# Optimization experiments

Hardware: AMD Instinct MI355X
Metric: run time of the kernel (lower is better)

The kernel has to match this reference:

```python
import jax, jax.numpy as jnp
import numpy as np

N = 16384      # batch (samples / graph nodes)
H = 256        # hid_dim
PRED_LEN = 24


def setup_inputs() -> dict:
    key = jax.random.key(0)
    ks = jax.random.split(key, 9)
    s = 1.0 / np.sqrt(H)  # PyTorch default init bound for GRUCell / Linear(H, 1)
    return {
        "encoder_out": jax.random.normal(ks[0], (N, H), dtype=jnp.float32),
        # input_proj = Linear(1, H): weight [H,1] flattened to [H], bound 1/sqrt(1)=1
        "w_proj": jax.random.uniform(ks[1], (H,), jnp.float32, -1.0, 1.0),
        "b_proj": jax.random.uniform(ks[2], (H,), jnp.float32, -1.0, 1.0),
        # GRUCell weights: [3H, H] ordered (reset, update, new) as in PyTorch
        "W_ih": jax.random.uniform(ks[3], (3 * H, H), jnp.float32, -s, s),
        "b_ih": jax.random.uniform(ks[4], (3 * H,), jnp.float32, -s, s),
        "W_hh": jax.random.uniform(ks[5], (3 * H, H), jnp.float32, -s, s),
        "b_hh": jax.random.uniform(ks[6], (3 * H,), jnp.float32, -s, s),
        # output_layer = Linear(H, 1): weight [1,H] flattened to [H]
        "w_out": jax.random.uniform(ks[7], (H,), jnp.float32, -s, s),
        "b_out": jax.random.uniform(ks[8], (1,), jnp.float32, -s, s),
    }


def reference(encoder_out, w_proj, b_proj, W_ih, b_ih, W_hh, b_hh, w_out, b_out):
    def step(carry, _):
        h, x = carry                       # h: [N,H], x: [N,1] scalar step input
        px = x * w_proj + b_proj           # input_proj(Linear(1,H)) -> [N,H]
        gi = px @ W_ih.T + b_ih            # [N,3H]
        gh = h @ W_hh.T + b_hh             # [N,3H]
        i_r, i_z, i_n = jnp.split(gi, 3, axis=1)
        h_r, h_z, h_n = jnp.split(gh, 3, axis=1)
        r = jax.nn.sigmoid(i_r + h_r)
        z = jax.nn.sigmoid(i_z + h_z)
        n = jnp.tanh(i_n + r * h_n)
        h_new = (1.0 - z) * n + z * h      # PyTorch GRUCell update
        pred = (h_new @ w_out)[:, None] + b_out  # output_layer -> [N,1]
        next_x = jax.lax.stop_gradient(pred)     # matches pred_t.detach()
        return (h_new, next_x), pred[:, 0]

    x0 = jnp.zeros((encoder_out.shape[0], 1), dtype=encoder_out.dtype)  # start token
    _, preds = jax.lax.scan(step, (encoder_out, x0), None, length=PRED_LEN)
    return preds.T  # [N, pred_len]
```

## Files before the change

### kernel.cpp

```cpp
#include <hip/hip_runtime.h>
#include <hip/hip_bf16.h>

#define NS 16384
#define H 256
#define TH 768
#define PRED 24
#define LDA 272
#define WS_NEEDED (425984)

typedef short bf16x8 __attribute__((ext_vector_type(8)));
typedef float floatx4 __attribute__((ext_vector_type(4)));

__device__ __forceinline__ float b2f(unsigned short u) {
    return __uint_as_float(((unsigned int)u) << 16);
}
__device__ __forceinline__ unsigned short f2b(float f) {
    unsigned int u = __float_as_uint(f);
    return (unsigned short)((u + 0x7FFFu + ((u >> 16) & 1u)) >> 16);
}
__device__ __forceinline__ float fsig(float v) {
    return __builtin_amdgcn_rcpf(1.0f + __expf(-v));
}
__device__ __forceinline__ float ftanh(float v) {
    return 1.0f - 2.0f * __builtin_amdgcn_rcpf(1.0f + __expf(2.0f * v));
}

__global__ void prep_proj(const void* __restrict__ WihP, const void* __restrict__ wprojP,
                          const void* __restrict__ bprojP, const void* __restrict__ bihP,
                          const void* __restrict__ bhhP, const void* __restrict__ woutP,
                          const void* __restrict__ boutP,
                          float* __restrict__ u, float* __restrict__ c,
                          float* __restrict__ bhn, float* __restrict__ wo,
                          float* __restrict__ b0) {
    const int j = blockIdx.x;
    const int lane = threadIdx.x;
    unsigned long long bm = __ballot(!(fabsf(b2f(((const unsigned short*)WihP)[lane])) <= 0.25f));
    const bool f32in = (bm != 0ull);

    float su = 0.f, sc = 0.f;
    if (f32in) {
        const float* row = (const float*)WihP + (size_t)j * H;
        const float* wp = (const float*)wprojP;
        const float* bp = (const float*)bprojP;
        for (int k = lane; k < H; k += 64) {
            float w = row[k];
            su = fmaf(w, wp[k], su); sc = fmaf(w, bp[k], sc);
        }
    } else {
        const unsigned short* row = (const unsigned short*)WihP + (size_t)j * H;
        const unsigned short* wp = (const unsigned short*)wprojP;
        const unsigned short* bp = (const unsigned short*)bprojP;
        for (int k = lane; k < H; k += 64) {
            float w = b2f(row[k]);
            su = fmaf(w, b2f(wp[k]), su); sc = fmaf(w, b2f(bp[k]), sc);
        }
    }
    for (int m = 32; m; m >>= 1) { su += __shfl_xor(su, m, 64); sc += __shfl_xor(sc, m, 64); }

    if (lane == 0) {
        float bih = f32in ? ((const float*)bihP)[j] : b2f(((const unsigned short*)bihP)[j]);
        float bhh = f32in ? ((const float*)bhhP)[j] : b2f(((const unsigned short*)bhhP)[j]);
        u[j] = su;
        c[j] = sc + bih + (j < 512 ? bhh : 0.f);
        if (j >= 512) bhn[j - 512] = bhh;
    }
    if (j < H && lane == 1)
        wo[j] = f32in ? ((const float*)woutP)[j] : b2f(((const unsigned short*)woutP)[j]);
    if (j == 0 && lane == 2)
        b0[0] = f32in ? ((const float*)boutP)[0] : b2f(((const unsigned short*)boutP)[0]);
}

__global__ void prep_swz2(const void* __restrict__ WhhP, unsigned short* __restrict__ Wp) {
    const int cidx = blockIdx.x * 256 + threadIdx.x;
    unsigned long long bm = __ballot(!(fabsf(b2f(((const unsigned short*)WhhP)[threadIdx.x & 63])) <= 0.25f));
    const bool f32in = (bm != 0ull);

    const int lane = cidx & 63;
    const int fi   = cidx >> 6;
    const int s    = fi & 1;
    const int g    = (fi >> 1) % 3;
    const int kk   = ((fi >> 1) / 3) & 7;
    const int w    = (fi >> 1) / 24;
    const size_t src = (size_t)(g * 256 + s * 128 + w * 16 + (lane & 15)) * H
                     + kk * 32 + (lane >> 4) * 8;
    unsigned short* dst = Wp + (size_t)cidx * 8;
    if (f32in) {
        const float* sp = (const float*)WhhP + src;
#pragma unroll
        for (int e = 0; e < 8; ++e) dst[e] = f2b(sp[e]);
    } else {
        const unsigned short* sp = (const unsigned short*)WhhP + src;
#pragma unroll
        for (int e = 0; e < 8; ++e) dst[e] = sp[e];
    }
}

__global__ void prep_wof(const float* __restrict__ wo, unsigned short* __restrict__ wf) {
    const int idx = blockIdx.x * 256 + threadIdx.x;
    const int kk   = idx >> 9;
    const int lane = (idx >> 3) & 63;
    const int e    = idx & 7;
    unsigned short v = 0;
    if ((lane & 15) == 0) v = f2b(wo[kk * 32 + (lane >> 4) * 8 + e]);
    wf[idx] = v;
}

__global__ __launch_bounds__(512, 2)
void decode_wr2(const void* __restrict__ encP, const void* __restrict__ WihP,
                const unsigned short* __restrict__ Wp, const unsigned short* __restrict__ wf,
                const float* __restrict__ u, const float* __restrict__ c,
                const float* __restrict__ bhnA, const float* __restrict__ b0A,
                void* __restrict__ outP) {
    __shared__ __align__(16) unsigned short As[2][32 * LDA];
    __shared__ __align__(16) unsigned short Wl[8][6144];
    __shared__ __align__(16) unsigned short Wf[8 * 512];
    __shared__ float pred_out[32][PRED];
    __shared__ int sflag;

    const int tid  = threadIdx.x;
    const int w    = tid >> 6;
    const int lane = tid & 63;
    const int lo   = lane & 15;
    const int quad = lane >> 4;
    const int m0   = blockIdx.x * 32;

    if (tid == 0) sflag = 0;
    __syncthreads();
    if (!(fabsf(b2f(((const unsigned short*)WihP)[tid])) <= 0.25f)) sflag = 1;
    __syncthreads();
    const bool f32in = (sflag != 0);

    const float*          encF = (const float*)encP;
    const unsigned short* encB = (const unsigned short*)encP;

    for (int i = tid; i < 32 * H; i += 512) {
        int r = i >> 8, col = i & 255;
        float hv = f32in ? encF[(size_t)(m0 + r) * H + col] : b2f(encB[(size_t)(m0 + r) * H + col]);
        As[0][r * LDA + col] = f2b(hv);
    }
    for (int i = tid; i < 4096; i += 512) Wf[i] = wf[i];

    float ur[2], uz[2], un[2], cr[2], cz[2], cn[2], bh[2];
#pragma unroll
    for (int s = 0; s < 2; ++s) {
        const int jj = s * 128 + w * 16 + lo;
        ur[s] = u[jj];       uz[s] = u[256 + jj];       un[s] = u[512 + jj];
        cr[s] = c[jj];       cz[s] = c[256 + jj];       cn[s] = c[512 + jj];
        bh[s] = bhnA[jj];
    }
    const float b0 = b0A[0];

    const unsigned short* wp = Wp + (size_t)w * 24576 + lane * 8;
    bf16x8 bW[6][3][2];
#pragma unroll
    for (int kk = 0; kk < 6; ++kk)
#pragma unroll
        for (int g = 0; g < 3; ++g)
#pragma unroll
            for (int s = 0; s < 2; ++s)
                bW[kk][g][s] = *(const bf16x8*)(wp + (size_t)((kk * 3 + g) * 2 + s) * 512);
#pragma unroll
    for (int kk = 6; kk < 8; ++kk)
#pragma unroll
        for (int g = 0; g < 3; ++g)
#pragma unroll
            for (int s = 0; s < 2; ++s) {
                bf16x8 v = *(const bf16x8*)(wp + (size_t)((kk * 3 + g) * 2 + s) * 512);
                *(bf16x8*)&Wl[w][(((kk - 6) * 3 + g) * 2 + s) * 512 + lane * 8] = v;
            }
    __syncthreads();

    int p = 0;
#pragma unroll 1
    for (int t = 0; t < PRED; ++t) {
        floatx4 acc[3][2][2];
        floatx4 woacc[2];
#pragma unroll
        for (int g = 0; g < 3; ++g)
#pragma unroll
            for (int s = 0; s < 2; ++s)
#pragma unroll
                for (int im = 0; im < 2; ++im) acc[g][s][im] = (floatx4){0.f, 0.f, 0.f, 0.f};
        woacc[0] = (floatx4){0.f, 0.f, 0.f, 0.f};
        woacc[1] = (floatx4){0.f, 0.f, 0.f, 0.f};

        const unsigned short* Ap = As[p];
        unsigned short*       An = As[p ^ 1];

#pragma unroll
        for (int kk = 0; kk < 8; ++kk) {
            bf16x8 a[2];
#pragma unroll
            for (int im = 0; im < 2; ++im)
                a[im] = *(const bf16x8*)&Ap[(im * 16 + lo) * LDA + kk * 32 + quad * 8];
            bf16x8 bwv = *(const bf16x8*)&Wf[kk * 512 + lane * 8];
            if (kk < 6) {
#pragma unroll
                for (int g = 0; g < 3; ++g)
#pragma unroll
                    for (int s = 0; s < 2; ++s)
#pragma unroll
                        for (int im = 0; im < 2; ++im)
                            acc[g][s][im] = __builtin_amdgcn_mfma_f32_16x16x32_bf16(
                                a[im], bW[kk][g][s], acc[g][s][im], 0, 0, 0);
            } else {
                bf16x8 b[3][2];
#pragma unroll
                for (int g = 0; g < 3; ++g)
#pragma unroll
                    for (int s = 0; s < 2; ++s)
                        b[g][s] = *(const bf16x8*)&Wl[w][(((kk - 6) * 3 + g) * 2 + s) * 512 + lane * 8];
#pragma unroll
                for (int g = 0; g < 3; ++g)
#pragma unroll
                    for (int s = 0; s < 2; ++s)
#pragma unroll
                        for (int im = 0; im < 2; ++im)
                            acc[g][s][im] = __builtin_amdgcn_mfma_f32_16x16x32_bf16(
                                a[im], b[g][s], acc[g][s][im], 0, 0, 0);
            }
#pragma unroll
            for (int im = 0; im < 2; ++im)
                woacc[im] = __builtin_amdgcn_mfma_f32_16x16x32_bf16(a[im], bwv, woacc[im], 0, 0, 0);
        }

#pragma unroll
        for (int im = 0; im < 2; ++im) {
#pragma unroll
            for (int v = 0; v < 4; ++v) {
                const int row = im * 16 + quad * 4 + v;
                float xv = 0.f;
                if (t > 0) xv = b0 + __shfl(woacc[im][v], quad << 4, 64);
#pragma unroll
                for (int s = 0; s < 2; ++s) {
                    const int jj = s * 128 + w * 16 + lo;
                    const int hofs = row * LDA + jj;
                    const float hold = b2f(Ap[hofs]);
                    float r  = fsig(fmaf(xv, ur[s], cr[s]) + acc[0][s][im][v]);
                    float z  = fsig(fmaf(xv, uz[s], cz[s]) + acc[1][s][im][v]);
                    float n  = ftanh(fmaf(xv, un[s], cn[s]) + r * (acc[2][s][im][v] + bh[s]));
                    float hn = fmaf(z, hold - n, n);
                    An[hofs] = f2b(hn);
                }
                if (w == 0 && lo == 0 && t > 0) pred_out[row][t - 1] = xv;
            }
        }
        __syncthreads();
        p ^= 1;
    }

    if (w == 0) {
        const unsigned short* Ap = As[p];
        floatx4 wa[2];
        wa[0] = (floatx4){0.f, 0.f, 0.f, 0.f};
        wa[1] = (floatx4){0.f, 0.f, 0.f, 0.f};
#pragma unroll
        for (int kk = 0; kk < 8; ++kk) {
            bf16x8 bwv = *(const bf16x8*)&Wf[kk * 512 + lane * 8];
#pragma unroll
            for (int im = 0; im < 2; ++im) {
                bf16x8 a = *(const bf16x8*)&Ap[(im * 16 + lo) * LDA + kk * 32 + quad * 8];
                wa[im] = __builtin_amdgcn_mfma_f32_16x16x32_bf16(a, bwv, wa[im], 0, 0, 0);
            }
        }
        if (lo == 0) {
#pragma unroll
            for (int im = 0; im < 2; ++im)
#pragma unroll
                for (int v = 0; v < 4; ++v)
                    pred_out[im * 16 + quad * 4 + v][PRED - 1] = b0 + wa[im][v];
        }
    }
    __syncthreads();

    for (int i = tid; i < 32 * PRED; i += 512) {
        int row = i / PRED, tt = i % PRED;
        float pr = pred_out[row][tt];
        if (f32in) ((float*)outP)[(size_t)(m0 + row) * PRED + tt] = pr;
        else ((unsigned short*)outP)[(size_t)(m0 + row) * PRED + tt] = f2b(pr);
    }
}

__global__ __launch_bounds__(512, 2)
void decode_all(const void* __restrict__ encP,   const void* __restrict__ wprojP,
                const void* __restrict__ bprojP, const void* __restrict__ WihP,
                const void* __restrict__ bihP,   const void* __restrict__ WhhP,
                const void* __restrict__ bhhP,   const void* __restrict__ woutP,
                const void* __restrict__ boutP,  void* __restrict__ outP) {
    __shared__ __align__(16) unsigned short Asf[64 * LDA];
    __shared__ float u_lds[TH], c_lds[TH];
    __shared__ float bhn_lds[H], wo_lds[H];
    __shared__ float wp_lds[H], bp_lds[H];
    __shared__ float pred_lds[2][64];
    __shared__ int sflag;

    const int tid  = threadIdx.x;
    const int wid  = tid >> 6;
    const int lane = tid & 63;
    const int lo   = lane & 15;
    const int quad = lane >> 4;
    const int rh   = wid & 3;
    const int ch   = wid >> 2;
    const int m0   = blockIdx.x * 64;

    if (tid == 0) sflag = 0;
    __syncthreads();
    if (!(fabsf(b2f(((const unsigned short*)WihP)[tid])) <= 0.25f)) sflag = 1;
    __syncthreads();
    const bool f32in = (sflag != 0);

    const float*          encF = (const float*)encP;
    const unsigned short* encB = (const unsigned short*)encP;
    const unsigned short* WhhB = (const unsigned short*)WhhP;
    const float*          WhhF = (const float*)WhhP;

    if (tid < H) {
        wp_lds[tid] = f32in ? ((const float*)wprojP)[tid] : b2f(((const unsigned short*)wprojP)[tid]);
        bp_lds[tid] = f32in ? ((const float*)bprojP)[tid] : b2f(((const unsigned short*)bprojP)[tid]);
        wo_lds[tid] = f32in ? ((const float*)woutP)[tid]  : b2f(((const unsigned short*)woutP)[tid]);
    }
    __syncthreads();

    for (int j = tid; j < TH; j += 512) {
        float su = 0.f, sc = 0.f;
        if (f32in) {
            const float* row = (const float*)WihP + (size_t)j * H;
            for (int k = 0; k < H; ++k) { float w = row[k]; su = fmaf(w, wp_lds[k], su); sc = fmaf(w, bp_lds[k], sc); }
        } else {
            const unsigned short* row = (const unsigned short*)WihP + (size_t)j * H;
            for (int k = 0; k < H; ++k) { float w = b2f(row[k]); su = fmaf(w, wp_lds[k], su); sc = fmaf(w, bp_lds[k], sc); }
        }
        float bih = f32in ? ((const float*)bihP)[j] : b2f(((const unsigned short*)bihP)[j]);
        float bhh = f32in ? ((const float*)bhhP)[j] : b2f(((const unsigned short*)bhhP)[j]);
        u_lds[j] = su;
        c_lds[j] = sc + bih + (j < 512 ? bhh : 0.f);
        if (j >= 512) bhn_lds[j - 512] = bhh;
    }

    for (int i = tid; i < 64 * H; i += 512) {
        int r = i >> 8, col = i & 255;
        float hv = f32in ? encF[(size_t)(m0 + r) * H + col] : b2f(encB[(size_t)(m0 + r) * H + col]);
        Asf[r * LDA + col] = f2b(hv);
    }
    float hold[8][4];
#pragma unroll
    for (int s = 0; s < 8; ++s)
#pragma unroll
        for (int v = 0; v < 4; ++v) {
            int row = m0 + rh * 16 + quad * 4 + v;
            int jj  = ch * 128 + s * 16 + lo;
            hold[s][v] = f32in ? encF[(size_t)row * H + jj] : b2f(encB[(size_t)row * H + jj]);
        }
    const float b0 = f32in ? ((const float*)boutP)[0] : b2f(((const unsigned short*)boutP)[0]);

    float xm[4] = {0.f, 0.f, 0.f, 0.f};
    __syncthreads();

    const int aBase = (rh * 16 + lo) * LDA;
    const int wCol0 = ch * 128 + lo;

#pragma unroll 1
    for (int t = 0; t < PRED; ++t) {
        floatx4 acc[3][8];
#pragma unroll
        for (int g = 0; g < 3; ++g)
#pragma unroll
            for (int s = 0; s < 8; ++s) acc[g][s] = (floatx4){0.f, 0.f, 0.f, 0.f};

        if (f32in) {
#pragma unroll 1
            for (int kk = 0; kk < 8; ++kk) {
                bf16x8 a = *(const bf16x8*)&Asf[aBase + kk * 32 + quad * 8];
#pragma unroll
                for (int g = 0; g < 3; ++g)
#pragma unroll
                    for (int s = 0; s < 8; ++s) {
                        const float* wr = WhhF + (size_t)(g * 256 + wCol0 + s * 16) * H + kk * 32 + quad * 8;
                        float4 w0 = *(const float4*)wr;
                        float4 w1 = *(const float4*)(wr + 4);
                        bf16x8 b;
                        b[0] = (short)f2b(w0.x); b[1] = (short)f2b(w0.y);
                        b[2] = (short)f2b(w0.z); b[3] = (short)f2b(w0.w);
                        b[4] = (short)f2b(w1.x); b[5] = (short)f2b(w1.y);
                        b[6] = (short)f2b(w1.z); b[7] = (short)f2b(w1.w);
                        acc[g][s] = __builtin_amdgcn_mfma_f32_16x16x32_bf16(a, b, acc[g][s], 0, 0, 0);
                    }
            }
        } else {
#pragma unroll 1
            for (int kk = 0; kk < 8; ++kk) {
                bf16x8 a = *(const bf16x8*)&Asf[aBase + kk * 32 + quad * 8];
#pragma unroll
                for (int g = 0; g < 3; ++g)
#pragma unroll
                    for (int s = 0; s < 8; ++s) {
                        bf16x8 b = *(const bf16x8*)(WhhB + (size_t)(g * 256 + wCol0 + s * 16) * H + kk * 32 + quad * 8);
                        acc[g][s] = __builtin_amdgcn_mfma_f32_16x16x32_bf16(a, b, acc[g][s], 0, 0, 0);
                    }
            }
        }
        __syncthreads();

        float pp[4] = {0.f, 0.f, 0.f, 0.f};
#pragma unroll
        for (int s = 0; s < 8; ++s) {
            const int jj = ch * 128 + s * 16 + lo;
            const float urr = u_lds[jj], uzz = u_lds[256 + jj], unn = u_lds[512 + jj];
            const float crr = c_lds[jj], czz = c_lds[256 + jj], cnn = c_lds[512 + jj];
            const float bhn = bhn_lds[jj], wovv = wo_lds[jj];
#pragma unroll
            for (int v = 0; v < 4; ++v) {
                const float xv = xm[v];
                float r  = fsig(fmaf(xv, urr, crr) + acc[0][s][v]);
                float z  = fsig(fmaf(xv, uzz, czz) + acc[1][s][v]);
                float n  = ftanh(fmaf(xv, unn, cnn) + r * (acc[2][s][v] + bhn));
                float hn = fmaf(z, hold[s][v] - n, n);
                hold[s][v] = hn;
                Asf[(rh * 16 + quad * 4 + v) * LDA + jj] = f2b(hn);
                pp[v] = fmaf(hn, wovv, pp[v]);
            }
        }
#pragma unroll
        for (int v = 0; v < 4; ++v) {
            float pv = pp[v];
            pv += __shfl_xor(pv, 1, 64);
            pv += __shfl_xor(pv, 2, 64);
            pv += __shfl_xor(pv, 4, 64);
            pv += __shfl_xor(pv, 8, 64);
            if (lo == 0) pred_lds[ch][rh * 16 + quad * 4 + v] = pv;
        }
        __syncthreads();

#pragma unroll
        for (int v = 0; v < 4; ++v) {
            const int ml = rh * 16 + quad * 4 + v;
            xm[v] = b0 + pred_lds[0][ml] + pred_lds[1][ml];
        }
        if (tid < 64) {
            float pr = b0 + pred_lds[0][tid] + pred_lds[1][tid];
            if (f32in) ((float*)outP)[(size_t)(m0 + tid) * PRED + t] = pr;
            else ((unsigned short*)outP)[(size_t)(m0 + tid) * PRED + t] = f2b(pr);
        }
    }
}

extern "C" void kernel_launch(void* const* d_in, const int* in_sizes, int n_in,
                              void* d_out, int out_size, void* d_ws, size_t ws_size,
                              hipStream_t stream) {
    if (ws_size >= (size_t)WS_NEEDED) {
        char* ws = (char*)d_ws;
        unsigned short* Wp = (unsigned short*)ws;
        float* u   = (float*)(ws + 393216);
        float* c   = (float*)(ws + 396288);
        float* bhn = (float*)(ws + 399360);
        float* wo  = (float*)(ws + 400384);
        float* b0  = (float*)(ws + 401408);
        unsigned short* wf = (unsigned short*)(ws + 402432);
        prep_proj<<<TH, 64, 0, stream>>>(d_in[3], d_in[1], d_in[2], d_in[4], d_in[6],
                                         d_in[7], d_in[8], u, c, bhn, wo, b0);
        prep_swz2<<<96, 256, 0, stream>>>(d_in[5], Wp);
        prep_wof<<<16, 256, 0, stream>>>(wo, wf);
        decode_wr2<<<NS / 32, 512, 0, stream>>>(d_in[0], d_in[3], Wp, wf, u, c, bhn, b0, d_out);
    } else {
        decode_all<<<NS / 64, 512, 0, stream>>>(d_in[0], d_in[1], d_in[2], d_in[3],
                                                d_in[4], d_in[5], d_in[6], d_in[7],
                                                d_in[8], d_out);
    }
}
```

Baseline: 319.9 us.

## Hold all W_hh in registers with 64-row tiles and fp32 hidden state

The decode kernel now processes 64 rows per block instead of 32 and runs one block per CU. It keeps the full swizzled W_hh slice and the output-weight fragments in registers rather than splitting them between registers and LDS. The previous hidden state is carried in fp32 registers instead of being re-read from the bf16 LDS tile. This doubles the MFMA reuse of each weight fragment and removes the LDS weight traffic, at the cost of heavy register pressure, lower occupancy and only 256 blocks on the device.

```diff
diff --git a/kernel.cpp b/kernel.cpp
--- a/kernel.cpp
+++ b/kernel.cpp
@@ -105,16 +105,14 @@
     wf[idx] = v;
 }
 
-__global__ __launch_bounds__(512, 2)
-void decode_wr2(const void* __restrict__ encP, const void* __restrict__ WihP,
-                const unsigned short* __restrict__ Wp, const unsigned short* __restrict__ wf,
-                const float* __restrict__ u, const float* __restrict__ c,
-                const float* __restrict__ bhnA, const float* __restrict__ b0A,
-                void* __restrict__ outP) {
-    __shared__ __align__(16) unsigned short As[2][32 * LDA];
-    __shared__ __align__(16) unsigned short Wl[8][6144];
-    __shared__ __align__(16) unsigned short Wf[8 * 512];
-    __shared__ float pred_out[32][PRED];
+__global__ __launch_bounds__(512, 1)
+void decode_wf(const void* __restrict__ encP, const void* __restrict__ WihP,
+               const unsigned short* __restrict__ Wp, const unsigned short* __restrict__ wf,
+               const float* __restrict__ u, const float* __restrict__ c,
+               const float* __restrict__ bhnA, const float* __restrict__ b0A,
+               void* __restrict__ outP) {
+    __shared__ __align__(16) unsigned short As[2][64 * LDA];
+    __shared__ float pred_out[64][PRED];
     __shared__ int sflag;
 
     const int tid  = threadIdx.x;
@@ -122,7 +120,7 @@
     const int lane = tid & 63;
     const int lo   = lane & 15;
     const int quad = lane >> 4;
-    const int m0   = blockIdx.x * 32;
+    const int m0   = blockIdx.x * 64;
 
     if (tid == 0) sflag = 0;
     __syncthreads();
@@ -133,12 +131,11 @@
     const float*          encF = (const float*)encP;
     const unsigned short* encB = (const unsigned short*)encP;
 
-    for (int i = tid; i < 32 * H; i += 512) {
+    for (int i = tid; i < 64 * H; i += 512) {
         int r = i >> 8, col = i & 255;
         float hv = f32in ? encF[(size_t)(m0 + r) * H + col] : b2f(encB[(size_t)(m0 + r) * H + col]);
         As[0][r * LDA + col] = f2b(hv);
     }
-    for (int i = tid; i < 4096; i += 512) Wf[i] = wf[i];
 
     float ur[2], uz[2], un[2], cr[2], cz[2], cn[2], bh[2];
 #pragma unroll
@@ -150,82 +147,73 @@
     }
     const float b0 = b0A[0];
 
+    float hold[4][4][2];
+#pragma unroll
+    for (int im = 0; im < 4; ++im)
+#pragma unroll
+        for (int v = 0; v < 4; ++v)
+#pragma unroll
+            for (int s = 0; s < 2; ++s) {
+                int row = m0 + im * 16 + quad * 4 + v;
+                int jj  = s * 128 + w * 16 + lo;
+                hold[im][v][s] = f32in ? encF[(size_t)row * H + jj]
+                                       : b2f(encB[(size_t)row * H + jj]);
+            }
+
     const unsigned short* wp = Wp + (size_t)w * 24576 + lane * 8;
-    bf16x8 bW[6][3][2];
-#pragma unroll
-    for (int kk = 0; kk < 6; ++kk)
+    bf16x8 bW[8][3][2];
+#pragma unroll
+    for (int kk = 0; kk < 8; ++kk)
 #pragma unroll
         for (int g = 0; g < 3; ++g)
 #pragma unroll
             for (int s = 0; s < 2; ++s)
                 bW[kk][g][s] = *(const bf16x8*)(wp + (size_t)((kk * 3 + g) * 2 + s) * 512);
-#pragma unroll
-    for (int kk = 6; kk < 8; ++kk)
-#pragma unroll
-        for (int g = 0; g < 3; ++g)
-#pragma unroll
-            for (int s = 0; s < 2; ++s) {
-                bf16x8 v = *(const bf16x8*)(wp + (size_t)((kk * 3 + g) * 2 + s) * 512);
-                *(bf16x8*)&Wl[w][(((kk - 6) * 3 + g) * 2 + s) * 512 + lane * 8] = v;
-            }
+    bf16x8 bWo[8];
+#pragma unroll
+    for (int kk = 0; kk < 8; ++kk)
+        bWo[kk] = *(const bf16x8*)(wf + kk * 512 + lane * 8);
+
     __syncthreads();
 
     int p = 0;
 #pragma unroll 1
     for (int t = 0; t < PRED; ++t) {
-        floatx4 acc[3][2][2];
-        floatx4 woacc[2];
+        floatx4 acc[3][2][4];
+        floatx4 woacc[4];
 #pragma unroll
         for (int g = 0; g < 3; ++g)
 #pragma unroll
             for (int s = 0; s < 2; ++s)
 #pragma unroll
-                for (int im = 0; im < 2; ++im) acc[g][s][im] = (floatx4){0.f, 0.f, 0.f, 0.f};
-        woacc[0] = (floatx4){0.f, 0.f, 0.f, 0.f};
-        woacc[1] = (floatx4){0.f, 0.f, 0.f, 0.f};
+                for (int im = 0; im < 4; ++im) acc[g][s][im] = (floatx4){0.f, 0.f, 0.f, 0.f};
+#pragma unroll
+        for (int im = 0; im < 4; ++im) woacc[im] = (floatx4){0.f, 0.f, 0.f, 0.f};
 
         const unsigned short* Ap = As[p];
         unsigned short*       An = As[p ^ 1];
 
 #pragma unroll
         for (int kk = 0; kk < 8; ++kk) {
-            bf16x8 a[2];
-#pragma unroll
-            for (int im = 0; im < 2; ++im)
+            bf16x8 a[4];
+#pragma unroll
+            for (int im = 0; im < 4; ++im)
                 a[im] = *(const bf16x8*)&Ap[(im * 16 + lo) * LDA + kk * 32 + quad * 8];
-            bf16x8 bwv = *(const bf16x8*)&Wf[kk * 512 + lane * 8];
-            if (kk < 6) {
-#pragma unroll
-                for (int g = 0; g < 3; ++g)
-#pragma unroll
-                    for (int s = 0; s < 2; ++s)
-#pragma unroll
-                        for (int im = 0; im < 2; ++im)
-                            acc[g][s][im] = __builtin_amdgcn_mfma_f32_16x16x32_bf16(
-                                a[im], bW[kk][g][s], acc[g][s][im], 0, 0, 0);
-            } else {
-                bf16x8 b[3][2];
-#pragma unroll
-                for (int g = 0; g < 3; ++g)
-#pragma unroll
-                    for (int s = 0; s < 2; ++s)
-                        b[g][s] = *(const bf16x8*)&Wl[w][(((kk - 6) * 3 + g) * 2 + s) * 512 + lane * 8];
-#pragma unroll
-                for (int g = 0; g < 3; ++g)
-#pragma unroll
-                    for (int s = 0; s < 2; ++s)
-#pragma unroll
-                        for (int im = 0; im < 2; ++im)
-                            acc[g][s][im] = __builtin_amdgcn_mfma_f32_16x16x32_bf16(
-                                a[im], b[g][s], acc[g][s][im], 0, 0, 0);
-            }
-#pragma unroll
-            for (int im = 0; im < 2; ++im)
-                woacc[im] = __builtin_amdgcn_mfma_f32_16x16x32_bf16(a[im], bwv, woacc[im], 0, 0, 0);
-        }
-
-#pragma unroll
-        for (int im = 0; im < 2; ++im) {
+#pragma unroll
+            for (int g = 0; g < 3; ++g)
+#pragma unroll
+                for (int s = 0; s < 2; ++s)
+#pragma unroll
+                    for (int im = 0; im < 4; ++im)
+                        acc[g][s][im] = __builtin_amdgcn_mfma_f32_16x16x32_bf16(
+                            a[im], bW[kk][g][s], acc[g][s][im], 0, 0, 0);
+#pragma unroll
+            for (int im = 0; im < 4; ++im)
+                woacc[im] = __builtin_amdgcn_mfma_f32_16x16x32_bf16(a[im], bWo[kk], woacc[im], 0, 0, 0);
+        }
+
+#pragma unroll
+        for (int im = 0; im < 4; ++im) {
 #pragma unroll
             for (int v = 0; v < 4; ++v) {
                 const int row = im * 16 + quad * 4 + v;
@@ -234,13 +222,12 @@
 #pragma unroll
                 for (int s = 0; s < 2; ++s) {
                     const int jj = s * 128 + w * 16 + lo;
-                    const int hofs = row * LDA + jj;
-                    const float hold = b2f(Ap[hofs]);
                     float r  = fsig(fmaf(xv, ur[s], cr[s]) + acc[0][s][im][v]);
                     float z  = fsig(fmaf(xv, uz[s], cz[s]) + acc[1][s][im][v]);
                     float n  = ftanh(fmaf(xv, un[s], cn[s]) + r * (acc[2][s][im][v] + bh[s]));
-                    float hn = fmaf(z, hold - n, n);
-                    An[hofs] = f2b(hn);
+                    float hn = fmaf(z, hold[im][v][s] - n, n);
+                    hold[im][v][s] = hn;
+                    An[row * LDA + jj] = f2b(hn);
                 }
                 if (w == 0 && lo == 0 && t > 0) pred_out[row][t - 1] = xv;
             }
@@ -251,21 +238,20 @@
 
     if (w == 0) {
         const unsigned short* Ap = As[p];
-        floatx4 wa[2];
-        wa[0] = (floatx4){0.f, 0.f, 0.f, 0.f};
-        wa[1] = (floatx4){0.f, 0.f, 0.f, 0.f};
+        floatx4 wa[4];
+#pragma unroll
+        for (int im = 0; im < 4; ++im) wa[im] = (floatx4){0.f, 0.f, 0.f, 0.f};
 #pragma unroll
         for (int kk = 0; kk < 8; ++kk) {
-            bf16x8 bwv = *(const bf16x8*)&Wf[kk * 512 + lane * 8];
-#pragma unroll
-            for (int im = 0; im < 2; ++im) {
+#pragma unroll
+            for (int im = 0; im < 4; ++im) {
                 bf16x8 a = *(const bf16x8*)&Ap[(im * 16 + lo) * LDA + kk * 32 + quad * 8];
-                wa[im] = __builtin_amdgcn_mfma_f32_16x16x32_bf16(a, bwv, wa[im], 0, 0, 0);
+                wa[im] = __builtin_amdgcn_mfma_f32_16x16x32_bf16(a, bWo[kk], wa[im], 0, 0, 0);
             }
         }
         if (lo == 0) {
 #pragma unroll
-            for (int im = 0; im < 2; ++im)
+            for (int im = 0; im < 4; ++im)
 #pragma unroll
                 for (int v = 0; v < 4; ++v)
                     pred_out[im * 16 + quad * 4 + v][PRED - 1] = b0 + wa[im][v];
@@ -273,7 +259,7 @@
     }
     __syncthreads();
 
-    for (int i = tid; i < 32 * PRED; i += 512) {
+    for (int i = tid; i < 64 * PRED; i += 512) {
         int row = i / PRED, tt = i % PRED;
         float pr = pred_out[row][tt];
         if (f32in) ((float*)outP)[(size_t)(m0 + row) * PRED + tt] = pr;
@@ -460,7 +446,7 @@
                                          d_in[7], d_in[8], u, c, bhn, wo, b0);
         prep_swz2<<<96, 256, 0, stream>>>(d_in[5], Wp);
         prep_wof<<<16, 256, 0, stream>>>(wo, wf);
-        decode_wr2<<<NS / 32, 512, 0, stream>>>(d_in[0], d_in[3], Wp, wf, u, c, bhn, b0, d_out);
+        decode_wf<<<NS / 64, 512, 0, stream>>>(d_in[0], d_in[3], Wp, wf, u, c, bhn, b0, d_out);
     } else {
         decode_all<<<NS / 64, 512, 0, stream>>>(d_in[0], d_in[1], d_in[2], d_in[3],
                                                 d_in[4], d_in[5], d_in[6], d_in[7],
```

Result: slower. 643.9 us (+101.3%).
